# Kernel tuning notes

Measured on AMD Instinct MI355X. Metric: run time of the kernel, lower is better.

The kernel has to match this reference:

```python
import jax, jax.numpy as jnp
import numpy as np

NGROUPS = 368
NMODELS = 16
BATCH = 16384

def setup_inputs() -> dict:
    key = jax.random.key(0)
    kx, kw, kb = jax.random.split(key, 3)
    x = jax.random.normal(kx, (BATCH, NGROUPS, NMODELS), dtype=jnp.float32)
    # 368 independent Linear(nmodels, 1): weight [368, nmodels], bias [368]
    bound = 1.0 / np.sqrt(NMODELS)
    W = jax.random.uniform(kw, (NGROUPS, NMODELS), minval=-bound, maxval=bound, dtype=jnp.float32)
    b = jax.random.uniform(kb, (NGROUPS,), minval=-bound, maxval=bound, dtype=jnp.float32)
    return {"x": x, "W": W, "b": b}

def reference(x, W, b):
    # Fused grouped dot: out[bg] = sum_n x[b,g,n] * W[g,n] + b[g]
    return jnp.einsum("bgn,gn->bg", x, W) + b
```

## Files before the change

kernel.cpp:

```cpp
#include <hip/hip_runtime.h>


#define NGROUPS 368

__global__ __launch_bounds__(256) void ensemble_kernel(
    const float4* __restrict__ x4,
    const float4* __restrict__ w4,
    const float* __restrict__ bias,
    float* __restrict__ out,
    int totf4)
{
    const int tid    = blockIdx.x * 256 + threadIdx.x;
    const int stride = gridDim.x * 256;
    const int q      = tid & 3;

    #pragma unroll 4
    for (int f = tid; f < totf4; f += stride) {
        const float4 xv = x4[f];
        const int o = f >> 2;
        const int g = o % NGROUPS;
        const float4 wv = w4[(g << 2) | q];

        float s = xv.x * wv.x + xv.y * wv.y + xv.z * wv.z + xv.w * wv.w;
        s += __shfl_xor(s, 1);
        s += __shfl_xor(s, 2);

        if (q == 0) {
            out[o] = s + bias[g];
        }
    }
}

extern "C" void kernel_launch(void* const* d_in, const int* in_sizes, int n_in,
                              void* d_out, int out_size, void* d_ws, size_t ws_size,
                              hipStream_t stream)
{
    const float4* x4   = (const float4*)d_in[0];
    const float4* w4   = (const float4*)d_in[1];
    const float* bias  = (const float*)d_in[2];
    float* out = (float*)d_out;

    const int totf4 = in_sizes[0] >> 2;

    int blocks = (totf4 + 255) / 256;
    if (blocks > 2048) blocks = 2048;

    ensemble_kernel<<<blocks, 256, 0, stream>>>(x4, w4, bias, out, totf4);
}
```

Measured before the change: 89.02 us.

## Compute one output per thread with four nontemporal vector loads

Replaces the grid-stride loop, where four lanes cooperate via shuffles on one output, with a one-output-per-thread kernel that loads all 16 inputs as four nontemporal float4 loads. It launches one thread per output instead of capping the grid, and uses a nontemporal store for the result. The aim is to remove the shuffle reduction and the redundant lane work, and to keep more memory requests in flight. The trade-off is that adjacent lanes now access addresses 64 bytes apart per load instruction, which reduces coalescing within each instruction.

```diff
diff --git a/kernel.cpp b/kernel.cpp
--- a/kernel.cpp
+++ b/kernel.cpp
@@ -3,47 +3,50 @@
 
 #define NGROUPS 368
 
+typedef float vfloat4 __attribute__((ext_vector_type(4)));
+
 __global__ __launch_bounds__(256) void ensemble_kernel(
-    const float4* __restrict__ x4,
-    const float4* __restrict__ w4,
+    const vfloat4* __restrict__ x4,
+    const vfloat4* __restrict__ w4,
     const float* __restrict__ bias,
     float* __restrict__ out,
-    int totf4)
+    int total)
 {
-    const int tid    = blockIdx.x * 256 + threadIdx.x;
-    const int stride = gridDim.x * 256;
-    const int q      = tid & 3;
+    const int o = blockIdx.x * 256 + threadIdx.x;
+    if (o >= total) return;
 
-    #pragma unroll 4
-    for (int f = tid; f < totf4; f += stride) {
-        const float4 xv = x4[f];
-        const int o = f >> 2;
-        const int g = o % NGROUPS;
-        const float4 wv = w4[(g << 2) | q];
+    const int g = o % NGROUPS;
 
-        float s = xv.x * wv.x + xv.y * wv.y + xv.z * wv.z + xv.w * wv.w;
-        s += __shfl_xor(s, 1);
-        s += __shfl_xor(s, 2);
+    const vfloat4* xp = x4 + ((size_t)o << 2);
+    const vfloat4 x0 = __builtin_nontemporal_load(xp + 0);
+    const vfloat4 x1 = __builtin_nontemporal_load(xp + 1);
+    const vfloat4 x2 = __builtin_nontemporal_load(xp + 2);
+    const vfloat4 x3 = __builtin_nontemporal_load(xp + 3);
 
-        if (q == 0) {
-            out[o] = s + bias[g];
-        }
-    }
+    const vfloat4 w0 = w4[(g << 2) + 0];
+    const vfloat4 w1 = w4[(g << 2) + 1];
+    const vfloat4 w2 = w4[(g << 2) + 2];
+    const vfloat4 w3 = w4[(g << 2) + 3];
+
+    float s = x0.x * w0.x + x0.y * w0.y + x0.z * w0.z + x0.w * w0.w;
+    s += x1.x * w1.x + x1.y * w1.y + x1.z * w1.z + x1.w * w1.w;
+    s += x2.x * w2.x + x2.y * w2.y + x2.z * w2.z + x2.w * w2.w;
+    s += x3.x * w3.x + x3.y * w3.y + x3.z * w3.z + x3.w * w3.w;
+
+    __builtin_nontemporal_store(s + bias[g], out + o);
 }
 
 extern "C" void kernel_launch(void* const* d_in, const int* in_sizes, int n_in,
                               void* d_out, int out_size, void* d_ws, size_t ws_size,
                               hipStream_t stream)
 {
-    const float4* x4   = (const float4*)d_in[0];
-    const float4* w4   = (const float4*)d_in[1];
+    const vfloat4* x4  = (const vfloat4*)d_in[0];
+    const vfloat4* w4  = (const vfloat4*)d_in[1];
     const float* bias  = (const float*)d_in[2];
     float* out = (float*)d_out;
 
-    const int totf4 = in_sizes[0] >> 2;
+    const int total = out_size;
+    const int blocks = (total + 255) / 256;
 
-    int blocks = (totf4 + 255) / 256;
-    if (blocks > 2048) blocks = 2048;
-
-    ensemble_kernel<<<blocks, 256, 0, stream>>>(x4, w4, bias, out, totf4);
+    ensemble_kernel<<<blocks, 256, 0, stream>>>(x4, w4, bias, out, total);
 }
```

After: 120.1 us. +34.9%, slower.
